# Kernel tuning notes

Hardware: AMD Instinct MI355X
Metric: run time of the kernel (lower is better)

The kernel has to match this reference:

```python
import jax, jax.numpy as jnp
import numpy as np

L2_REG = 0.02


def setup_inputs() -> dict:
    key = jax.random.key(0)
    k1, k2 = jax.random.split(key)
    n, d = 4096, 1024
    anchors = jax.random.normal(k1, (n, d), dtype=jnp.float32)
    positives = jax.random.normal(k2, (n, d), dtype=jnp.float32)
    return {"anchors": anchors, "positives": positives}


def reference(anchors, positives):
    # Fused equivalent of the per-row masked_select loop:
    # x[i, j] = a_i . (p_j - p_i) = S[i, j] - S[i, i], for j != i
    n = anchors.shape[0]
    S = anchors @ positives.T                     # (n, n)
    x = S - jnp.diag(S)[:, None]                  # subtract anchor-positive sim per row
    offdiag = ~jnp.eye(n, dtype=bool)
    # sum over negatives j != i of exp(x[i, j])
    s = jnp.sum(jnp.where(offdiag, jnp.exp(x), 0.0), axis=1)  # (n,)
    n_pair = jnp.mean(jnp.log1p(s))
    l2 = jnp.sum(anchors ** 2 + positives ** 2) / n
    return n_pair + L2_REG * l2
```

## Files before the change

kernel.cpp:

```cpp
#include <hip/hip_runtime.h>
#include <math.h>
#include <stdint.h>

#define N 4096
#define Dm 1024
#define BM 128
#define BN 128
#define BK 64
#define NCB (N / 64)

typedef __attribute__((ext_vector_type(8))) short bf16x8;
typedef __attribute__((ext_vector_type(4))) float f32x4;

typedef const void __attribute__((address_space(1)))* gas_t;
typedef void __attribute__((address_space(3)))* las_t;

static __device__ __forceinline__ void gload_lds16(const void* g, void* l) {
    __builtin_amdgcn_global_load_lds((gas_t)g, (las_t)l, 16, 0, 0);
}

static __device__ __forceinline__ unsigned short f2bf(float f) {
    unsigned int u = __float_as_uint(f);
    unsigned int r = (u + 0x7fff + ((u >> 16) & 1)) >> 16;
    return (unsigned short)r;
}

__global__ __launch_bounds__(256) void prep_kernel(const float* __restrict__ A,
                                                   const float* __restrict__ P,
                                                   unsigned short* __restrict__ Abf,
                                                   unsigned short* __restrict__ Pbf,
                                                   float* __restrict__ D,
                                                   float* __restrict__ rowl2) {
    int row = blockIdx.x;
    int t = threadIdx.x;
    const float4* a4 = (const float4*)(A + (size_t)row * Dm);
    const float4* p4 = (const float4*)(P + (size_t)row * Dm);
    float4 a = a4[t], p = p4[t];
    ushort4 ab, pb;
    ab.x = f2bf(a.x); ab.y = f2bf(a.y); ab.z = f2bf(a.z); ab.w = f2bf(a.w);
    pb.x = f2bf(p.x); pb.y = f2bf(p.y); pb.z = f2bf(p.z); pb.w = f2bf(p.w);
    ((ushort4*)(Abf + (size_t)row * Dm))[t] = ab;
    ((ushort4*)(Pbf + (size_t)row * Dm))[t] = pb;
    float dot = a.x * p.x + a.y * p.y + a.z * p.z + a.w * p.w;
    float l2  = a.x * a.x + a.y * a.y + a.z * a.z + a.w * a.w
              + p.x * p.x + p.y * p.y + p.z * p.z + p.w * p.w;
#pragma unroll
    for (int off = 32; off; off >>= 1) {
        dot += __shfl_xor(dot, off, 64);
        l2  += __shfl_xor(l2,  off, 64);
    }
    __shared__ float sd[4], sl[4];
    int wave = t >> 6;
    if ((t & 63) == 0) { sd[wave] = dot; sl[wave] = l2; }
    __syncthreads();
    if (t == 0) {
        D[row]     = sd[0] + sd[1] + sd[2] + sd[3];
        rowl2[row] = sl[0] + sl[1] + sl[2] + sl[3];
    }
}

__global__ __launch_bounds__(256) void npair_mfma(const unsigned short* __restrict__ Abf,
                                                  const unsigned short* __restrict__ Pbf,
                                                  const float* __restrict__ D,
                                                  float* __restrict__ Mpart,
                                                  float* __restrict__ Spart) {
    __shared__ unsigned short At[BM * BK];
    __shared__ unsigned short Bt[BN * BK];
    __shared__ float Ds[BM];
    int tid = threadIdx.x;
    int wid = tid >> 6, lane = tid & 63;
    int wr = wid >> 1, wc = wid & 1;
    int row0 = blockIdx.y * BM, col0 = blockIdx.x * BN;

    const unsigned short* gA[4]; const unsigned short* gB[4];
    unsigned short* lA[4]; unsigned short* lB[4];
#pragma unroll
    for (int b = 0; b < 4; ++b) {
        int L = b * 256 + tid;
        int row = L >> 3, c = L & 7;
        int kch = c ^ (row & 7);
        gA[b] = Abf + (size_t)(row0 + row) * Dm + (kch << 3);
        gB[b] = Pbf + (size_t)(col0 + row) * Dm + (kch << 3);
        lA[b] = At + (size_t)L * 8;
        lB[b] = Bt + (size_t)L * 8;
    }
    if (tid < BM) Ds[tid] = D[row0 + tid];

    f32x4 acc[4][4] = {};

    for (int kt = 0; kt < Dm; kt += BK) {
        __syncthreads();
#pragma unroll
        for (int b = 0; b < 4; ++b) {
            gload_lds16(gA[b] + kt, lA[b]);
            gload_lds16(gB[b] + kt, lB[b]);
        }
        __syncthreads();
#pragma unroll
        for (int ks = 0; ks < 2; ++ks) {
            bf16x8 af[4], bfr[4];
#pragma unroll
            for (int i = 0; i < 4; ++i) {
                int g = (ks << 2) + (lane >> 4);
                int arow = wr * 64 + i * 16 + (lane & 15);
                af[i]  = *(const bf16x8*)(At + arow * BK + ((g ^ (arow & 7)) << 3));
                int brow = wc * 64 + i * 16 + (lane & 15);
                bfr[i] = *(const bf16x8*)(Bt + brow * BK + ((g ^ (brow & 7)) << 3));
            }
#pragma unroll
            for (int i = 0; i < 4; ++i)
#pragma unroll
                for (int j = 0; j < 4; ++j)
                    acc[i][j] = __builtin_amdgcn_mfma_f32_16x16x32_bf16(af[i], bfr[j], acc[i][j], 0, 0, 0);
        }
    }

    int cb = blockIdx.x * 2 + wc;
#pragma unroll
    for (int rt = 0; rt < 4; ++rt) {
        int rloc = wr * 64 + rt * 16 + ((lane >> 4) << 2);
#pragma unroll
        for (int e = 0; e < 4; ++e) {
            int gr = row0 + rloc + e;
            float Dv = Ds[rloc + e];
            float xs[4];
            float m = -INFINITY;
#pragma unroll
            for (int ct = 0; ct < 4; ++ct) {
                int gc = col0 + wc * 64 + ct * 16 + (lane & 15);
                float x = acc[rt][ct][e] - Dv;
                if (gr == gc) x = -INFINITY;
                xs[ct] = x;
                m = fmaxf(m, x);
            }
#pragma unroll
            for (int off = 8; off; off >>= 1) m = fmaxf(m, __shfl_xor(m, off, 64));
            float s = 0.0f;
#pragma unroll
            for (int ct = 0; ct < 4; ++ct) s += __expf(xs[ct] - m);
#pragma unroll
            for (int off = 8; off; off >>= 1) s += __shfl_xor(s, off, 64);
            if ((lane & 15) == 0) {
                Mpart[(size_t)gr * NCB + cb] = m;
                Spart[(size_t)gr * NCB + cb] = s;
            }
        }
    }
}

__global__ __launch_bounds__(256) void combine_rows(const float* __restrict__ Mpart,
                                                    const float* __restrict__ Spart,
                                                    float* __restrict__ loss) {
    int t = threadIdx.x;
    int lane = t & 63;
    int row = blockIdx.x * 4 + (t >> 6);
    float mp = Mpart[(size_t)row * NCB + lane];
    float sp = Spart[(size_t)row * NCB + lane];
    float m = mp;
#pragma unroll
    for (int off = 32; off; off >>= 1) m = fmaxf(m, __shfl_xor(m, off, 64));
    float s = sp * __expf(mp - m);
#pragma unroll
    for (int off = 32; off; off >>= 1) s += __shfl_xor(s, off, 64);
    if (lane == 0) loss[row] = m + logf(__expf(-m) + s);
}

__global__ __launch_bounds__(256) void final_reduce(const float* __restrict__ loss,
                                                    const float* __restrict__ rowl2,
                                                    float* __restrict__ out) {
    int t = threadIdx.x;
    float accL = 0.0f, acc2 = 0.0f;
    for (int i = t; i < N; i += 256) {
        accL += loss[i];
        acc2 += rowl2[i];
    }
#pragma unroll
    for (int off = 32; off; off >>= 1) {
        accL += __shfl_xor(accL, off, 64);
        acc2 += __shfl_xor(acc2, off, 64);
    }
    __shared__ float sa[4], sb[4];
    int wave = t >> 6;
    if ((t & 63) == 0) { sa[wave] = accL; sb[wave] = acc2; }
    __syncthreads();
    if (t == 0) {
        float L  = sa[0] + sa[1] + sa[2] + sa[3];
        float l2 = sb[0] + sb[1] + sb[2] + sb[3];
        out[0] = L / (float)N + 0.02f * (l2 / (float)N);
    }
}

extern "C" void kernel_launch(void* const* d_in, const int* in_sizes, int n_in,
                              void* d_out, int out_size, void* d_ws, size_t ws_size,
                              hipStream_t stream) {
    const float* A = (const float*)d_in[0];
    const float* P = (const float*)d_in[1];
    float* out = (float*)d_out;

    unsigned short* Abf = (unsigned short*)d_ws;
    unsigned short* Pbf = Abf + (size_t)N * Dm;
    float* D     = (float*)(Pbf + (size_t)N * Dm);
    float* rowl2 = D + N;
    float* loss  = rowl2 + N;
    float* Mpart = loss + N;
    float* Spart = Mpart + (size_t)N * NCB;

    prep_kernel<<<N, 256, 0, stream>>>(A, P, Abf, Pbf, D, rowl2);
    dim3 grid(N / BN, N / BM);
    npair_mfma<<<grid, 256, 0, stream>>>(Abf, Pbf, D, Mpart, Spart);
    combine_rows<<<N / 4, 256, 0, stream>>>(Mpart, Spart, loss);
    final_reduce<<<1, 256, 0, stream>>>(loss, rowl2, out);
}
```

Before: 132.1 us.

## Switch GEMM operands from bf16 to fp8 using scaled MFMA 16x16x128

```diff
diff --git a/kernel.cpp b/kernel.cpp
--- a/kernel.cpp
+++ b/kernel.cpp
@@ -6,10 +6,11 @@
 #define Dm 1024
 #define BM 128
 #define BN 128
-#define BK 64
+#define BK 128
 #define NCB (N / 64)
 
-typedef __attribute__((ext_vector_type(8))) short bf16x8;
+typedef __attribute__((ext_vector_type(8))) int   i32x8;
+typedef __attribute__((ext_vector_type(4))) int   i32x4;
 typedef __attribute__((ext_vector_type(4))) float f32x4;
 
 typedef const void __attribute__((address_space(1)))* gas_t;
@@ -19,16 +20,10 @@
     __builtin_amdgcn_global_load_lds((gas_t)g, (las_t)l, 16, 0, 0);
 }
 
-static __device__ __forceinline__ unsigned short f2bf(float f) {
-    unsigned int u = __float_as_uint(f);
-    unsigned int r = (u + 0x7fff + ((u >> 16) & 1)) >> 16;
-    return (unsigned short)r;
-}
-
 __global__ __launch_bounds__(256) void prep_kernel(const float* __restrict__ A,
                                                    const float* __restrict__ P,
-                                                   unsigned short* __restrict__ Abf,
-                                                   unsigned short* __restrict__ Pbf,
+                                                   unsigned char* __restrict__ Af8,
+                                                   unsigned char* __restrict__ Pf8,
                                                    float* __restrict__ D,
                                                    float* __restrict__ rowl2) {
     int row = blockIdx.x;
@@ -36,11 +31,13 @@
     const float4* a4 = (const float4*)(A + (size_t)row * Dm);
     const float4* p4 = (const float4*)(P + (size_t)row * Dm);
     float4 a = a4[t], p = p4[t];
-    ushort4 ab, pb;
-    ab.x = f2bf(a.x); ab.y = f2bf(a.y); ab.z = f2bf(a.z); ab.w = f2bf(a.w);
-    pb.x = f2bf(p.x); pb.y = f2bf(p.y); pb.z = f2bf(p.z); pb.w = f2bf(p.w);
-    ((ushort4*)(Abf + (size_t)row * Dm))[t] = ab;
-    ((ushort4*)(Pbf + (size_t)row * Dm))[t] = pb;
+    int pa = 0, pp = 0;
+    pa = __builtin_amdgcn_cvt_pk_fp8_f32(a.x, a.y, pa, false);
+    pa = __builtin_amdgcn_cvt_pk_fp8_f32(a.z, a.w, pa, true);
+    pp = __builtin_amdgcn_cvt_pk_fp8_f32(p.x, p.y, pp, false);
+    pp = __builtin_amdgcn_cvt_pk_fp8_f32(p.z, p.w, pp, true);
+    ((int*)(Af8 + (size_t)row * Dm))[t] = pa;
+    ((int*)(Pf8 + (size_t)row * Dm))[t] = pp;
     float dot = a.x * p.x + a.y * p.y + a.z * p.z + a.w * p.w;
     float l2  = a.x * a.x + a.y * a.y + a.z * a.z + a.w * a.w
               + p.x * p.x + p.y * p.y + p.z * p.z + p.w * p.w;
@@ -59,30 +56,30 @@
     }
 }
 
-__global__ __launch_bounds__(256) void npair_mfma(const unsigned short* __restrict__ Abf,
-                                                  const unsigned short* __restrict__ Pbf,
+__global__ __launch_bounds__(256) void npair_mfma(const unsigned char* __restrict__ Af8,
+                                                  const unsigned char* __restrict__ Pf8,
                                                   const float* __restrict__ D,
                                                   float* __restrict__ Mpart,
                                                   float* __restrict__ Spart) {
-    __shared__ unsigned short At[BM * BK];
-    __shared__ unsigned short Bt[BN * BK];
+    __shared__ unsigned char At[BM * BK];
+    __shared__ unsigned char Bt[BN * BK];
     __shared__ float Ds[BM];
     int tid = threadIdx.x;
     int wid = tid >> 6, lane = tid & 63;
     int wr = wid >> 1, wc = wid & 1;
     int row0 = blockIdx.y * BM, col0 = blockIdx.x * BN;
 
-    const unsigned short* gA[4]; const unsigned short* gB[4];
-    unsigned short* lA[4]; unsigned short* lB[4];
+    const unsigned char* gA[4]; const unsigned char* gB[4];
+    unsigned char* lA[4]; unsigned char* lB[4];
 #pragma unroll
     for (int b = 0; b < 4; ++b) {
         int L = b * 256 + tid;
         int row = L >> 3, c = L & 7;
         int kch = c ^ (row & 7);
-        gA[b] = Abf + (size_t)(row0 + row) * Dm + (kch << 3);
-        gB[b] = Pbf + (size_t)(col0 + row) * Dm + (kch << 3);
-        lA[b] = At + (size_t)L * 8;
-        lB[b] = Bt + (size_t)L * 8;
+        gA[b] = Af8 + (size_t)(row0 + row) * Dm + (kch << 4);
+        gB[b] = Pf8 + (size_t)(col0 + row) * Dm + (kch << 4);
+        lA[b] = At + (size_t)L * 16;
+        lB[b] = Bt + (size_t)L * 16;
     }
     if (tid < BM) Ds[tid] = D[row0 + tid];
 
@@ -96,22 +93,32 @@
             gload_lds16(gB[b] + kt, lB[b]);
         }
         __syncthreads();
-#pragma unroll
-        for (int ks = 0; ks < 2; ++ks) {
-            bf16x8 af[4], bfr[4];
-#pragma unroll
-            for (int i = 0; i < 4; ++i) {
-                int g = (ks << 2) + (lane >> 4);
-                int arow = wr * 64 + i * 16 + (lane & 15);
-                af[i]  = *(const bf16x8*)(At + arow * BK + ((g ^ (arow & 7)) << 3));
-                int brow = wc * 64 + i * 16 + (lane & 15);
-                bfr[i] = *(const bf16x8*)(Bt + brow * BK + ((g ^ (brow & 7)) << 3));
-            }
+
+        int c0 = (lane >> 4) << 1;
+        i32x8 af[4];
+#pragma unroll
+        for (int i = 0; i < 4; ++i) {
+            int arow = wr * 64 + i * 16 + (lane & 15);
+            i32x4 lo = *(const i32x4*)(At + arow * BK + (((c0    ) ^ (arow & 7)) << 4));
+            i32x4 hi = *(const i32x4*)(At + arow * BK + (((c0 + 1) ^ (arow & 7)) << 4));
+            af[i][0] = lo[0]; af[i][1] = lo[1]; af[i][2] = lo[2]; af[i][3] = lo[3];
+            af[i][4] = hi[0]; af[i][5] = hi[1]; af[i][6] = hi[2]; af[i][7] = hi[3];
+        }
+#pragma unroll
+        for (int j = 0; j < 4; ++j) {
+            int brow = wc * 64 + j * 16 + (lane & 15);
+            i32x4 lo = *(const i32x4*)(Bt + brow * BK + (((c0    ) ^ (brow & 7)) << 4));
+            i32x4 hi = *(const i32x4*)(Bt + brow * BK + (((c0 + 1) ^ (brow & 7)) << 4));
+            i32x8 bf;
+            bf[0] = lo[0]; bf[1] = lo[1]; bf[2] = lo[2]; bf[3] = lo[3];
+            bf[4] = hi[0]; bf[5] = hi[1]; bf[6] = hi[2]; bf[7] = hi[3];
 #pragma unroll
             for (int i = 0; i < 4; ++i)
-#pragma unroll
-                for (int j = 0; j < 4; ++j)
-                    acc[i][j] = __builtin_amdgcn_mfma_f32_16x16x32_bf16(af[i], bfr[j], acc[i][j], 0, 0, 0);
+                acc[i][j] = __builtin_amdgcn_mfma_scale_f32_16x16x128_f8f6f4(
+                    af[i], bf, acc[i][j],
+                    0, 0,
+                    0, 127,
+                    0, 127);
         }
     }
 
@@ -197,17 +204,17 @@
     const float* P = (const float*)d_in[1];
     float* out = (float*)d_out;
 
-    unsigned short* Abf = (unsigned short*)d_ws;
-    unsigned short* Pbf = Abf + (size_t)N * Dm;
-    float* D     = (float*)(Pbf + (size_t)N * Dm);
+    unsigned char* Af8 = (unsigned char*)d_ws;
+    unsigned char* Pf8 = Af8 + (size_t)N * Dm;
+    float* D     = (float*)(Pf8 + (size_t)N * Dm);
     float* rowl2 = D + N;
     float* loss  = rowl2 + N;
     float* Mpart = loss + N;
     float* Spart = Mpart + (size_t)N * NCB;
 
-    prep_kernel<<<N, 256, 0, stream>>>(A, P, Abf, Pbf, D, rowl2);
+    prep_kernel<<<N, 256, 0, stream>>>(A, P, Af8, Pf8, D, rowl2);
     dim3 grid(N / BN, N / BM);
-    npair_mfma<<<grid, 256, 0, stream>>>(Abf, Pbf, D, Mpart, Spart);
+    npair_mfma<<<grid, 256, 0, stream>>>(Af8, Pf8, D, Mpart, Spart);
     combine_rows<<<N / 4, 256, 0, stream>>>(Mpart, Spart, loss);
     final_reduce<<<1, 256, 0, stream>>>(loss, rowl2, out);
 }
```

After: 137.5 us. +4.1%, slower.

## Register-prefetch next K tile and fuse row combine with final reduction

Applied to the files above, without the earlier changes.

```diff
diff --git a/kernel.cpp b/kernel.cpp
--- a/kernel.cpp
+++ b/kernel.cpp
@@ -10,14 +10,8 @@
 #define NCB (N / 64)
 
 typedef __attribute__((ext_vector_type(8))) short bf16x8;
+typedef __attribute__((ext_vector_type(4))) int   i32x4;
 typedef __attribute__((ext_vector_type(4))) float f32x4;
-
-typedef const void __attribute__((address_space(1)))* gas_t;
-typedef void __attribute__((address_space(3)))* las_t;
-
-static __device__ __forceinline__ void gload_lds16(const void* g, void* l) {
-    __builtin_amdgcn_global_load_lds((gas_t)g, (las_t)l, 16, 0, 0);
-}
 
 static __device__ __forceinline__ unsigned short f2bf(float f) {
     unsigned int u = __float_as_uint(f);
@@ -30,9 +24,11 @@
                                                    unsigned short* __restrict__ Abf,
                                                    unsigned short* __restrict__ Pbf,
                                                    float* __restrict__ D,
-                                                   float* __restrict__ rowl2) {
+                                                   float* __restrict__ rowl2,
+                                                   float* __restrict__ accum) {
     int row = blockIdx.x;
     int t = threadIdx.x;
+    if (row == 0 && t < 3) accum[t] = 0.0f;
     const float4* a4 = (const float4*)(A + (size_t)row * Dm);
     const float4* p4 = (const float4*)(P + (size_t)row * Dm);
     float4 a = a4[t], p = p4[t];
@@ -78,24 +74,37 @@
     for (int b = 0; b < 4; ++b) {
         int L = b * 256 + tid;
         int row = L >> 3, c = L & 7;
-        int kch = c ^ (row & 7);
-        gA[b] = Abf + (size_t)(row0 + row) * Dm + (kch << 3);
-        gB[b] = Pbf + (size_t)(col0 + row) * Dm + (kch << 3);
-        lA[b] = At + (size_t)L * 8;
-        lB[b] = Bt + (size_t)L * 8;
+        gA[b] = Abf + (size_t)(row0 + row) * Dm + (c << 3);
+        gB[b] = Pbf + (size_t)(col0 + row) * Dm + (c << 3);
+        int sw = c ^ (row & 7);
+        lA[b] = At + (size_t)row * BK + (sw << 3);
+        lB[b] = Bt + (size_t)row * BK + (sw << 3);
     }
     if (tid < BM) Ds[tid] = D[row0 + tid];
 
     f32x4 acc[4][4] = {};
+    i32x4 ra[4], rb[4];
+#pragma unroll
+    for (int b = 0; b < 4; ++b) {
+        ra[b] = *(const i32x4*)gA[b];
+        rb[b] = *(const i32x4*)gB[b];
+    }
 
     for (int kt = 0; kt < Dm; kt += BK) {
         __syncthreads();
 #pragma unroll
         for (int b = 0; b < 4; ++b) {
-            gload_lds16(gA[b] + kt, lA[b]);
-            gload_lds16(gB[b] + kt, lB[b]);
+            *(i32x4*)lA[b] = ra[b];
+            *(i32x4*)lB[b] = rb[b];
         }
         __syncthreads();
+        if (kt + BK < Dm) {
+#pragma unroll
+            for (int b = 0; b < 4; ++b) {
+                ra[b] = *(const i32x4*)(gA[b] + kt + BK);
+                rb[b] = *(const i32x4*)(gB[b] + kt + BK);
+            }
+        }
 #pragma unroll
         for (int ks = 0; ks < 2; ++ks) {
             bf16x8 af[4], bfr[4];
@@ -148,12 +157,14 @@
     }
 }
 
-__global__ __launch_bounds__(256) void combine_rows(const float* __restrict__ Mpart,
-                                                    const float* __restrict__ Spart,
-                                                    float* __restrict__ loss) {
+__global__ __launch_bounds__(256) void combine_final(const float* __restrict__ Mpart,
+                                                     const float* __restrict__ Spart,
+                                                     const float* __restrict__ rowl2,
+                                                     float* __restrict__ accum,
+                                                     float* __restrict__ out) {
     int t = threadIdx.x;
-    int lane = t & 63;
-    int row = blockIdx.x * 4 + (t >> 6);
+    int lane = t & 63, w = t >> 6;
+    int row = blockIdx.x * 4 + w;
     float mp = Mpart[(size_t)row * NCB + lane];
     float sp = Spart[(size_t)row * NCB + lane];
     float m = mp;
@@ -162,31 +173,23 @@
     float s = sp * __expf(mp - m);
 #pragma unroll
     for (int off = 32; off; off >>= 1) s += __shfl_xor(s, off, 64);
-    if (lane == 0) loss[row] = m + logf(__expf(-m) + s);
-}
-
-__global__ __launch_bounds__(256) void final_reduce(const float* __restrict__ loss,
-                                                    const float* __restrict__ rowl2,
-                                                    float* __restrict__ out) {
-    int t = threadIdx.x;
-    float accL = 0.0f, acc2 = 0.0f;
-    for (int i = t; i < N; i += 256) {
-        accL += loss[i];
-        acc2 += rowl2[i];
-    }
-#pragma unroll
-    for (int off = 32; off; off >>= 1) {
-        accL += __shfl_xor(accL, off, 64);
-        acc2 += __shfl_xor(acc2, off, 64);
-    }
-    __shared__ float sa[4], sb[4];
-    int wave = t >> 6;
-    if ((t & 63) == 0) { sa[wave] = accL; sb[wave] = acc2; }
+    __shared__ float ls[4];
+    if (lane == 0) ls[w] = m + logf(__expf(-m) + s);
     __syncthreads();
     if (t == 0) {
-        float L  = sa[0] + sa[1] + sa[2] + sa[3];
-        float l2 = sb[0] + sb[1] + sb[2] + sb[3];
-        out[0] = L / (float)N + 0.02f * (l2 / (float)N);
+        int r4 = blockIdx.x * 4;
+        float L = ls[0] + ls[1] + ls[2] + ls[3];
+        float R = rowl2[r4] + rowl2[r4 + 1] + rowl2[r4 + 2] + rowl2[r4 + 3];
+        atomicAdd(&accum[0], L);
+        atomicAdd(&accum[1], R);
+        __threadfence();
+        unsigned int old = atomicAdd((unsigned int*)&accum[2], 1u);
+        if (old == (unsigned int)(gridDim.x - 1)) {
+            __threadfence();
+            float Lt = atomicAdd(&accum[0], 0.0f);
+            float Rt = atomicAdd(&accum[1], 0.0f);
+            out[0] = Lt / (float)N + 0.02f * (Rt / (float)N);
+        }
     }
 }
 
@@ -201,13 +204,12 @@
     unsigned short* Pbf = Abf + (size_t)N * Dm;
     float* D     = (float*)(Pbf + (size_t)N * Dm);
     float* rowl2 = D + N;
-    float* loss  = rowl2 + N;
-    float* Mpart = loss + N;
+    float* accum = rowl2 + N;
+    float* Mpart = accum + 64;
     float* Spart = Mpart + (size_t)N * NCB;
 
-    prep_kernel<<<N, 256, 0, stream>>>(A, P, Abf, Pbf, D, rowl2);
+    prep_kernel<<<N, 256, 0, stream>>>(A, P, Abf, Pbf, D, rowl2, accum);
     dim3 grid(N / BN, N / BM);
     npair_mfma<<<grid, 256, 0, stream>>>(Abf, Pbf, D, Mpart, Spart);
-    combine_rows<<<N / 4, 256, 0, stream>>>(Mpart, Spart, loss);
-    final_reduce<<<1, 256, 0, stream>>>(loss, rowl2, out);
-}
+    combine_final<<<N / 4, 256, 0, stream>>>(Mpart, Spart, rowl2, accum, out);
+}
```

Result: slower. 169.1 us (+28.0%).

## Double-buffer LDS tiles with async prefetch and halve K tile

Applied to the files above, without the earlier changes.

```diff
diff --git a/kernel.cpp b/kernel.cpp
--- a/kernel.cpp
+++ b/kernel.cpp
@@ -6,7 +6,7 @@
 #define Dm 1024
 #define BM 128
 #define BN 128
-#define BK 64
+#define BK 32
 #define NCB (N / 64)
 
 typedef __attribute__((ext_vector_type(8))) short bf16x8;
@@ -64,55 +64,62 @@
                                                   const float* __restrict__ D,
                                                   float* __restrict__ Mpart,
                                                   float* __restrict__ Spart) {
-    __shared__ unsigned short At[BM * BK];
-    __shared__ unsigned short Bt[BN * BK];
+    __shared__ unsigned short At[2][BM * BK];
+    __shared__ unsigned short Bt[2][BN * BK];
     __shared__ float Ds[BM];
     int tid = threadIdx.x;
     int wid = tid >> 6, lane = tid & 63;
     int wr = wid >> 1, wc = wid & 1;
     int row0 = blockIdx.y * BM, col0 = blockIdx.x * BN;
 
-    const unsigned short* gA[4]; const unsigned short* gB[4];
-    unsigned short* lA[4]; unsigned short* lB[4];
-#pragma unroll
-    for (int b = 0; b < 4; ++b) {
+    const unsigned short* gA[2]; const unsigned short* gB[2];
+    int loff[2];
+#pragma unroll
+    for (int b = 0; b < 2; ++b) {
         int L = b * 256 + tid;
-        int row = L >> 3, c = L & 7;
-        int kch = c ^ (row & 7);
-        gA[b] = Abf + (size_t)(row0 + row) * Dm + (kch << 3);
-        gB[b] = Pbf + (size_t)(col0 + row) * Dm + (kch << 3);
-        lA[b] = At + (size_t)L * 8;
-        lB[b] = Bt + (size_t)L * 8;
+        int row = L >> 2, c = L & 3;
+        int g = c ^ ((row >> 1) & 3);
+        gA[b] = Abf + (size_t)(row0 + row) * Dm + (g << 3);
+        gB[b] = Pbf + (size_t)(col0 + row) * Dm + (g << 3);
+        loff[b] = L * 8;
     }
     if (tid < BM) Ds[tid] = D[row0 + tid];
 
     f32x4 acc[4][4] = {};
 
+#pragma unroll
+    for (int b = 0; b < 2; ++b) {
+        gload_lds16(gA[b], At[0] + loff[b]);
+        gload_lds16(gB[b], Bt[0] + loff[b]);
+    }
+
+    int p = 0;
     for (int kt = 0; kt < Dm; kt += BK) {
         __syncthreads();
-#pragma unroll
-        for (int b = 0; b < 4; ++b) {
-            gload_lds16(gA[b] + kt, lA[b]);
-            gload_lds16(gB[b] + kt, lB[b]);
+        if (kt + BK < Dm) {
+#pragma unroll
+            for (int b = 0; b < 2; ++b) {
+                gload_lds16(gA[b] + kt + BK, At[p ^ 1] + loff[b]);
+                gload_lds16(gB[b] + kt + BK, Bt[p ^ 1] + loff[b]);
+            }
         }
-        __syncthreads();
-#pragma unroll
-        for (int ks = 0; ks < 2; ++ks) {
-            bf16x8 af[4], bfr[4];
-#pragma unroll
-            for (int i = 0; i < 4; ++i) {
-                int g = (ks << 2) + (lane >> 4);
-                int arow = wr * 64 + i * 16 + (lane & 15);
-                af[i]  = *(const bf16x8*)(At + arow * BK + ((g ^ (arow & 7)) << 3));
-                int brow = wc * 64 + i * 16 + (lane & 15);
-                bfr[i] = *(const bf16x8*)(Bt + brow * BK + ((g ^ (brow & 7)) << 3));
-            }
-#pragma unroll
-            for (int i = 0; i < 4; ++i)
-#pragma unroll
-                for (int j = 0; j < 4; ++j)
-                    acc[i][j] = __builtin_amdgcn_mfma_f32_16x16x32_bf16(af[i], bfr[j], acc[i][j], 0, 0, 0);
+        const unsigned short* Ab = At[p];
+        const unsigned short* Bb = Bt[p];
+        bf16x8 af[4], bfr[4];
+        int g = lane >> 4;
+#pragma unroll
+        for (int i = 0; i < 4; ++i) {
+            int arow = wr * 64 + i * 16 + (lane & 15);
+            af[i]  = *(const bf16x8*)(Ab + arow * BK + ((g ^ ((arow >> 1) & 3)) << 3));
+            int brow = wc * 64 + i * 16 + (lane & 15);
+            bfr[i] = *(const bf16x8*)(Bb + brow * BK + ((g ^ ((brow >> 1) & 3)) << 3));
         }
+#pragma unroll
+        for (int i = 0; i < 4; ++i)
+#pragma unroll
+            for (int j = 0; j < 4; ++j)
+                acc[i][j] = __builtin_amdgcn_mfma_f32_16x16x32_bf16(af[i], bfr[j], acc[i][j], 0, 0, 0);
+        p ^= 1;
     }
 
     int cb = blockIdx.x * 2 + wc;
```

New measurement: 135.5 us. 2.6% more time.
